# Performance work log

Measured on AMD Instinct MI355X. Metric: run time of the kernel, lower is better.

Reference implementation:

```python
import jax, jax.numpy as jnp
import numpy as np

B, T, U, K, CDIM, S, M = 128, 600, 96, 10, 80, 512, 20
D1 = 3 + CDIM        # rnn1 input: x_t (3) + attention window w (CDIM)
D2 = 3 + S + CDIM    # rnn2 / rnn3 input: x_t + prev rnn out + w
OUT_DIM = 1 + 6 * M


def setup_inputs() -> dict:
    key = jax.random.key(0)
    ks = jax.random.split(key, 16)
    g = lambda k, shape: jax.random.normal(k, shape, jnp.float32) * 0.05
    z = lambda n: jnp.zeros((n,), jnp.float32)
    return {
        "x": jax.random.normal(ks[0], (B, T, 3), jnp.float32),
        "c_vec": jax.random.uniform(ks[1], (B, U, CDIM), jnp.float32),
        # FF cell 1 (input dim D1)
        "W_jx1": g(ks[2], (D1, S)), "b_jx1": z(S),
        "W_jh1": g(ks[3], (S, S)),  "b_jh1": z(S),
        "W_kx1": g(ks[4], (D1, S)), "b_kx1": z(S),
        "W_kh1": g(ks[5], (S, S)),  "b_kh1": z(S),
        # FF cell 2 (input dim D2) -- also used for the 3rd RNN (source reuses self.rnn2)
        "W_jx2": g(ks[6], (D2, S)), "b_jx2": z(S),
        "W_jh2": g(ks[7], (S, S)),  "b_jh2": z(S),
        "W_kx2": g(ks[8], (D2, S)), "b_kx2": z(S),
        "W_kh2": g(ks[9], (S, S)),  "b_kh2": z(S),
        # attention window head: S -> 3K
        "W_win": g(ks[10], (S, 3 * K)), "b_win": z(3 * K),
        # output head: S -> 1 + 6M
        "W_lin": g(ks[11], (S, OUT_DIM)), "b_lin": z(OUT_DIM),
    }


def _ff(inp, h, Wjx, bjx, Wjh, bjh, Wkx, bkx, Wkh, bkh):
    # custom gated cell: out = j*(1-h) + (1-k)*h
    j = jax.nn.sigmoid(inp @ Wjx + bjx + h @ Wjh + bjh)
    k = jax.nn.sigmoid(inp @ Wkx + bkx + h @ Wkh + bkh)
    return j * (1.0 - h) + (1.0 - k) * h


def reference(x, c_vec,
              W_jx1, b_jx1, W_jh1, b_jh1, W_kx1, b_kx1, W_kh1, b_kh1,
              W_jx2, b_jx2, W_jh2, b_jh2, W_kx2, b_kx2, W_kh2, b_kh2,
              W_win, b_win, W_lin, b_lin):
    u = jnp.arange(U, dtype=x.dtype)  # [U]

    def step(carry, xt):
        h1, h2, h3, kappa, w = carry  # h*: [B,S], kappa: [B,K], w: [B,CDIM]
        in1 = jnp.concatenate([xt, w], axis=-1)
        h1 = _ff(in1, h1, W_jx1, b_jx1, W_jh1, b_jh1, W_kx1, b_kx1, W_kh1, b_kh1)
        kg = h1 @ W_win + b_win                       # [B, 3K]
        a_hat, be_hat, k_hat = jnp.split(kg, 3, axis=1)
        alpha = jnp.exp(a_hat)                        # [B,K]
        beta = jnp.exp(be_hat)
        kappa = kappa + jnp.exp(k_hat)
        # phi[b,u] = sum_k alpha * exp(-beta * (kappa - u)^2)
        phi = jnp.sum(alpha[:, :, None] *
                      jnp.exp(-beta[:, :, None] * (kappa[:, :, None] - u) ** 2),
                      axis=1)                          # [B,U]
        w = jnp.einsum('bu,buc->bc', phi, c_vec)      # [B,CDIM]
        in2 = jnp.concatenate([xt, h1, w], axis=-1)
        h2 = _ff(in2, h2, W_jx2, b_jx2, W_jh2, b_jh2, W_kx2, b_kx2, W_kh2, b_kh2)
        in3 = jnp.concatenate([xt, h2, w], axis=-1)
        # source bug kept faithfully: third RNN reuses rnn2's weights
        h3 = _ff(in3, h3, W_jx2, b_jx2, W_jh2, b_jh2, W_kx2, b_kx2, W_kh2, b_kh2)
        return (h1, h2, h3, kappa, w), h3

    zS = jnp.zeros((B, S), x.dtype)
    init = (zS, zS, zS, jnp.zeros((B, K), x.dtype), jnp.zeros((B, CDIM), x.dtype))
    _, ys = jax.lax.scan(step, init, jnp.swapaxes(x, 0, 1))  # ys: [T,B,S]
    out_cat = jnp.swapaxes(ys, 0, 1).reshape(B * T, S)
    return out_cat @ W_lin + b_lin                    # [B*T, 1+6M]
```

## Files before the change

kernel.cpp:

```cpp
#include <hip/hip_runtime.h>
#include <hip/hip_bf16.h>

typedef __bf16 bf16;
typedef __bf16 bf16x8 __attribute__((ext_vector_type(8)));
typedef float  f32x4  __attribute__((ext_vector_type(4)));

#define AS1 __attribute__((address_space(1)))
#define AS3 __attribute__((address_space(3)))

#define NT   600
#define NB   128
#define NS   512
#define NU   96
#define NK   10
#define NC   80
#define NOUT 121

#define W1X_J 0
#define W1W_J 16384
#define W1H_J 65536
#define W1X_K 327680
#define W1W_K 344064
#define W1H_K 393216
#define W2X_J 655360
#define W2W_J 671744
#define W2A_J 720896
#define W2H_J 983040
#define W2X_K 1245184
#define W2W_K 1261568
#define W2A_K 1310720
#define W2H_K 1572864
#define WWIN  1835008
#define WLIN  1851392

#define BIAS_BYTE_OFF 3833856
#define H_BYTE_OFF    3842048
#define HBUF 65536
#define FLAG_BYTE_OFF 4659200
#define BAR_BYTE_OFF  4659264

#define HSTRIDE 520

#define AUX_SC0   1
#define AUX_SC0S1 17

__device__ __forceinline__ float ldIn(const void* q, long i, int isF32) {
  if (isF32) return ((const float*)q)[i];
  return (float)((const bf16*)q)[i];
}

struct KParams {
  const void* x;
  const void* c_vec;
  const void* b_win;
  const void* b_lin;
  const bf16* W;
  const float* bias;
  bf16* h1; bf16* h2; bf16* h3;
  void* out;
  const int* flag;
  int* bar;
};

template <int AUX>
__device__ __forceinline__ void stage_tile_async(const bf16* g, bf16* lds, int tid) {
  const int w = tid >> 6, lane = tid & 63;
#pragma unroll
  for (int r = 0; r < 4; ++r) {
    const int row = (w << 2) + r;
    __builtin_amdgcn_global_load_lds(
        (const AS1 void*)(g + (size_t)row * NS + (size_t)lane * 8),
        (AS3 void*)(lds + (size_t)row * HSTRIDE), 16, 0, AUX);
  }
}

__device__ __forceinline__ void group_arrive(int* gb) {
  __syncthreads();
  if (threadIdx.x == 0) {
    if ((__hip_atomic_fetch_add(gb, 1, __ATOMIC_RELAXED, __HIP_MEMORY_SCOPE_AGENT) & 31) == 31)
      __hip_atomic_fetch_add(gb + 8, 1, __ATOMIC_RELAXED, __HIP_MEMORY_SCOPE_AGENT);
  }
}
__device__ __forceinline__ void group_wait(int* gb, int target) {
  if (threadIdx.x == 0) {
    while (__hip_atomic_load(gb + 8, __ATOMIC_RELAXED, __HIP_MEMORY_SCOPE_AGENT) < target)
      __builtin_amdgcn_s_sleep(1);
  }
  __syncthreads();
  __atomic_signal_fence(__ATOMIC_ACQ_REL);
}

__device__ __forceinline__ void storeH(unsigned* dst, unsigned v, bool fast) {
  if (fast) *dst = v;
  else __hip_atomic_store(dst, v, __ATOMIC_RELAXED, __HIP_MEMORY_SCOPE_AGENT);
}

__global__ void sniff_kernel(const unsigned short* w, int* flag) {
  __shared__ int cnt;
  if (threadIdx.x == 0) cnt = 0;
  __syncthreads();
  int c = 0;
  for (int i = threadIdx.x; i < 8192; i += 256) {
    unsigned e = (w[2 * i] >> 7) & 0xFF;
    if (e == 0xFF || e < 96) c++;
  }
  atomicAdd(&cnt, c);
  __syncthreads();
  if (threadIdx.x == 0) *flag = (cnt > 512) ? 1 : 0;
}

__global__ void prep_kernel(const void* Wjx1, const void* Wjh1, const void* Wkx1, const void* Wkh1,
                            const void* Wjx2, const void* Wjh2, const void* Wkx2, const void* Wkh2,
                            const void* Wwin, const void* Wlin,
                            const void* bjx1, const void* bjh1, const void* bkx1, const void* bkh1,
                            const void* bjx2, const void* bjh2, const void* bkx2, const void* bkh2,
                            bf16* W, float* bias,
                            bf16* h1, bf16* h2, bf16* h3, int* bar,
                            const int* flag) {
  const int isF32 = *flag;
  const int r = blockIdx.y;
  const int e = blockIdx.x * 256 + threadIdx.x;
  if (r == 16) {
    if (e < 512) {
      bias[e]        = ldIn(bjx1, e, isF32) + ldIn(bjh1, e, isF32);
      bias[512 + e]  = ldIn(bkx1, e, isF32) + ldIn(bkh1, e, isF32);
      bias[1024 + e] = ldIn(bjx2, e, isF32) + ldIn(bjh2, e, isF32);
      bias[1536 + e] = ldIn(bkx2, e, isF32) + ldIn(bkh2, e, isF32);
    }
    return;
  }
  if (r == 17) {
    if (e < HBUF) {
      h1[e] = (bf16)0.f; h1[HBUF + e] = (bf16)0.f;
      h2[e] = (bf16)0.f; h2[HBUF + e] = (bf16)0.f;
      h3[e] = (bf16)0.f; h3[HBUF + e] = (bf16)0.f;
    }
    if (e < 1024) bar[e] = 0;
    return;
  }
  const int   row0s[16]  = {0,3,0, 0,3,0, 0,515,3,0, 0,515,3,0, 0,0};
  const int   klens[16]  = {3,80,512, 3,80,512, 3,80,512,512, 3,80,512,512, 512,512};
  const int   kpads[16]  = {32,96,512, 32,96,512, 32,96,512,512, 32,96,512,512, 512,512};
  const int   cpads[16]  = {512,512,512, 512,512,512, 512,512,512,512, 512,512,512,512, 32,128};
  const int   nsrcs[16]  = {512,512,512, 512,512,512, 512,512,512,512, 512,512,512,512, 30,121};
  const long  offs[16]   = {W1X_J,W1W_J,W1H_J, W1X_K,W1W_K,W1H_K,
                            W2X_J,W2W_J,W2A_J,W2H_J, W2X_K,W2W_K,W2A_K,W2H_K, WWIN,WLIN};
  const void* srcs[16]   = {Wjx1,Wjx1,Wjh1, Wkx1,Wkx1,Wkh1,
                            Wjx2,Wjx2,Wjx2,Wjh2, Wkx2,Wkx2,Wkx2,Wkh2, Wwin,Wlin};
  const int Kpad = kpads[r], cp = cpads[r];
  const long tot = (long)Kpad * cp;
  if (e >= tot) return;
  const int j    = e & 7;
  const int lane = (e >> 3) & 63;
  const int rest = e >> 9;
  const int kbs  = Kpad >> 5;
  const int kb   = rest % kbs;
  const int slab = rest / kbs;
  const int col  = slab * 16 + (lane & 15);
  const int k    = kb * 32 + ((lane >> 4) << 3) + j;
  const int Klen = klens[r], row0 = row0s[r], N = nsrcs[r];
  bf16 v = (bf16)0.f;
  if (k < Klen && col < N) v = (bf16)ldIn(srcs[r], (long)(row0 + k) * N + col, isF32);
  W[offs[r] + e] = v;
}

__device__ __forceinline__ void accum_term(f32x4& acc, int& cnt, int kh,
    const bf16* Arow, int astride, const bf16* B, int kbs,
    int lr, int ko, int lane) {
  for (int kb = 0; kb < kbs; ++kb) {
    if (((cnt++) & 1) != kh) continue;
    bf16x8 a = *(const bf16x8*)(Arow + (size_t)lr * astride + kb * 32 + ko);
    bf16x8 b = *(const bf16x8*)(B + ((size_t)kb * 64 + lane) * 8);
    acc = __builtin_amdgcn_mfma_f32_16x16x32_bf16(a, b, acc, 0, 0, 0);
  }
}

__device__ __forceinline__ void accStore(float* d, const f32x4& a) {
  d[0] = a[0]; d[1] = a[1]; d[2] = a[2]; d[3] = a[3];
}

__global__ __launch_bounds__(256) void scan_kernel(KParams p) {
  const int isF32 = *p.flag;
  const int tid  = threadIdx.x;
  const int wid  = tid >> 6;
  const int lane = tid & 63;
  const int wg   = blockIdx.x;
  const int m    = wg & 7;
  const int slab = wg >> 3;
  const int m16  = m << 4;
  const int lr   = lane & 15;
  const int ko   = (lane >> 4) << 3;
  const int g    = wid >> 1;
  const int kh   = wid & 1;

  unsigned* hg1w = (unsigned*)p.h1;
  unsigned* hg2w = (unsigned*)p.h2;
  unsigned* hg3w = (unsigned*)p.h3;

  __shared__ alignas(16) bf16 wLds[32768];
  __shared__ alignas(16) bf16 h1L[16 * HSTRIDE];
  __shared__ alignas(16) bf16 h2L[16 * HSTRIDE];
  __shared__ alignas(16) bf16 h3L[16 * HSTRIDE];
  __shared__ alignas(16) bf16 xtR[4][16][32];
  __shared__ alignas(16) bf16 wR[3][16][96];
  __shared__ float kapL[16][NK];
  __shared__ float alphaL[16][NK];
  __shared__ float betaL[16][NK];
  __shared__ float phiL[16][NU];
  __shared__ float accA[4][64][5];
  __shared__ float accB[4][64][5];
  __shared__ bf16  hOut1[16][16];
  __shared__ bf16  hOut2[16][16];
  __shared__ bf16  hOut3[16][16];

  for (int i = tid; i < 4 * 16 * 32; i += 256) (&xtR[0][0][0])[i] = (bf16)0.f;
  for (int i = tid; i < 3 * 16 * 96; i += 256) (&wR[0][0][0])[i] = (bf16)0.f;
  for (int i = tid; i < 16 * NK; i += 256) (&kapL[0][0])[i] = 0.f;

  const size_t oX2 = g ? W2X_K : W2X_J, oW2 = g ? W2W_K : W2W_J;
  const size_t oX1 = g ? W1X_K : W1X_J, oW1 = g ? W1W_K : W1W_J, oH1 = g ? W1H_K : W1H_J;
  const bf16* wA2 = wLds + (g ? 8192 : 0);
  const bf16* wH2 = wLds + (g ? 24576 : 16384);

  {
    const bf16* wsrc[4] = { p.W + W2A_J + (size_t)slab * (16 * NS),
                            p.W + W2A_K + (size_t)slab * (16 * NS),
                            p.W + W2H_J + (size_t)slab * (16 * NS),
                            p.W + W2H_K + (size_t)slab * (16 * NS) };
#pragma unroll
    for (int mt = 0; mt < 4; ++mt) {
#pragma unroll
      for (int r = 0; r < 4; ++r) {
        const int chunk = (wid << 2) + r;
        __builtin_amdgcn_global_load_lds(
            (const AS1 void*)(wsrc[mt] + chunk * 512 + lane * 8),
            (AS3 void*)(wLds + mt * 8192 + chunk * 512), 16, 0, 0);
      }
    }
  }
  if (tid < 48) {
    int row = tid / 3, d = tid - row * 3;
    xtR[0][row][d] = (bf16)ldIn(p.x, ((long)(m16 + row) * NT + 0) * 3 + d, isF32);
  }
  __syncthreads();

  int* gb = p.bar + m * 64;
  {
    int xcc = __builtin_amdgcn_s_getreg((3 << 11) | (0 << 6) | 20) & 31;
    if (tid == 0) {
      __hip_atomic_fetch_or((unsigned*)(gb + 32), 1u << xcc,
                            __ATOMIC_RELAXED, __HIP_MEMORY_SCOPE_AGENT);
      __threadfence();
      if ((__hip_atomic_fetch_add(gb + 16, 1, __ATOMIC_RELAXED, __HIP_MEMORY_SCOPE_AGENT) & 31) == 31)
        __hip_atomic_fetch_add(gb + 24, 1, __ATOMIC_RELAXED, __HIP_MEMORY_SCOPE_AGENT);
      while (__hip_atomic_load(gb + 24, __ATOMIC_RELAXED, __HIP_MEMORY_SCOPE_AGENT) < 1)
        __builtin_amdgcn_s_sleep(1);
    }
    __syncthreads();
  }
  const unsigned msk = __hip_atomic_load((unsigned*)(gb + 32),
                                         __ATOMIC_RELAXED, __HIP_MEMORY_SCOPE_AGENT);
  const bool fast = (msk & (msk - 1)) == 0;

  f32x4 acc2pre = {0.f, 0.f, 0.f, 0.f};
  int bt = 0;

  {
    f32x4 acc = {0.f, 0.f, 0.f, 0.f};
    int cnt = 0;
    accum_term(acc, cnt, kh, &xtR[0][0][0], 32, p.W + oX1 + (size_t)slab * NS,       1, lr, ko, lane);
    accum_term(acc, cnt, kh, &wR[0][0][0],  96, p.W + oW1 + (size_t)slab * (3 * NS), 3, lr, ko, lane);
    accStore(accB[wid][lane], acc);
    __syncthreads();
    {
      int ls = tid & 63, r = tid >> 6;
      int s = (slab << 4) + (ls & 15);
      int rowIdx = ((ls >> 4) << 2) + r;
      float jp = accB[0][ls][r] + accB[1][ls][r] + p.bias[0 + s];
      float jj = 1.f / (1.f + __expf(-jp));
      hOut1[rowIdx][ls & 15] = (bf16)jj;
    }
    __syncthreads();
    if (tid < 128) {
      int row = tid >> 3, c = tid & 7;
      union { unsigned u; unsigned short s[2]; } v;
      union { bf16 b; unsigned short s; } a0, a1;
      a0.b = hOut1[row][2 * c]; a1.b = hOut1[row][2 * c + 1];
      v.s[0] = a0.s; v.s[1] = a1.s;
      storeH(hg1w + (m16 + row) * 256 + slab * 8 + c, v.u, fast);
    }
    ++bt;
    group_arrive(gb);
    group_wait(gb, bt);
  }

  for (int i = 0; i <= NT + 2; ++i) {
    const bool A1  = (i <= NT - 1);
    const bool AF1 = (i <= NT - 2);
    const bool A2  = (i >= 1 && i <= NT);
    const bool A3  = (i >= 2 && i <= NT + 1);
    const bool AO  = (i >= 3) && (slab < 8);
    const bool APRE = (i <= NT - 1);

    if (i >= 1 && i <= NT + 1) {
      const bf16* g2 = p.h2 + (size_t)(i & 1) * HBUF + (size_t)m16 * NS;
      if (fast) stage_tile_async<AUX_SC0>(g2, h2L, tid);
      else      stage_tile_async<AUX_SC0S1>(g2, h2L, tid);
    }
    if (i >= 2) {
      const bf16* g3 = p.h3 + (size_t)((i + 1) & 1) * HBUF + (size_t)m16 * NS;
      if (fast) stage_tile_async<AUX_SC0>(g3, h3L, tid);
      else      stage_tile_async<AUX_SC0S1>(g3, h3L, tid);
    }
    if (i <= NT - 2 && tid < 48) {
      int row = tid / 3, d = tid - row * 3;
      xtR[(i + 1) & 3][row][d] = (bf16)ldIn(p.x, ((long)(m16 + row) * NT + (i + 1)) * 3 + d, isF32);
    }
    __syncthreads();

    if (A2) {
      f32x4 acc = acc2pre;
      int cnt = 20;
      accum_term(acc, cnt, kh, h2L, HSTRIDE, wH2, 16, lr, ko, lane);
      accStore(accA[wid][lane], acc);
    }
    if (AO) {
      f32x4 acc = {0.f, 0.f, 0.f, 0.f};
      const bf16* B = p.W + WLIN + (size_t)slab * (16 * NS);
      for (int kb = 0; kb < 16; ++kb) {
        if ((kb & 3) != wid) continue;
        bf16x8 a = *(const bf16x8*)(h3L + (size_t)lr * HSTRIDE + kb * 32 + ko);
        bf16x8 b = *(const bf16x8*)(B + ((size_t)kb * 64 + lane) * 8);
        acc = __builtin_amdgcn_mfma_f32_16x16x32_bf16(a, b, acc, 0, 0, 0);
      }
      accStore(accB[wid][lane], acc);
    }
    __syncthreads();

    if (A2) {
      int ls = tid & 63, r = tid >> 6;
      int s = (slab << 4) + (ls & 15);
      int rowIdx = ((ls >> 4) << 2) + r;
      float jp = accA[0][ls][r] + accA[1][ls][r] + p.bias[1024 + s];
      float kp = accA[2][ls][r] + accA[3][ls][r] + p.bias[1536 + s];
      float ho = (float)h2L[rowIdx * HSTRIDE + s];
      float jj = 1.f / (1.f + __expf(-jp));
      float kk = 1.f / (1.f + __expf(-kp));
      hOut2[rowIdx][ls & 15] = (bf16)(jj * (1.f - ho) + (1.f - kk) * ho);
    }
    if (AO && tid < 64) {
      int o = (slab << 4) + (tid & 15);
      if (o < NOUT) {
        float bl = ldIn(p.b_lin, o, isF32);
        int rb = (tid >> 4) << 2;
        for (int r = 0; r < 4; ++r) {
          float v = accB[0][tid][r] + accB[1][tid][r] + accB[2][tid][r] + accB[3][tid][r] + bl;
          long oi = ((long)(m16 + rb + r) * NT + (i - 3)) * NOUT + o;
          if (isF32) ((float*)p.out)[oi] = v; else ((bf16*)p.out)[oi] = (bf16)v;
        }
      }
    }
    __syncthreads();

    if (A3) {
      f32x4 acc = {0.f, 0.f, 0.f, 0.f};
      int cnt = 0;
      accum_term(acc, cnt, kh, &xtR[(i - 2) & 3][0][0], 32, p.W + oX2 + (size_t)slab * NS,      1,  lr, ko, lane);
      accum_term(acc, cnt, kh, h2L, HSTRIDE, wA2, 16, lr, ko, lane);
      accum_term(acc, cnt, kh, &wR[(i - 2) % 3][0][0], 96, p.W + oW2 + (size_t)slab * (3 * NS), 3,  lr, ko, lane);
      accum_term(acc, cnt, kh, h3L, HSTRIDE, wH2, 16, lr, ko, lane);
      accStore(accA[wid][lane], acc);
    }
    if (A2 && tid < 128) {
      int row = tid >> 3, c = tid & 7;
      union { unsigned u; unsigned short s[2]; } v;
      union { bf16 b; unsigned short s; } a0, a1;
      a0.b = hOut2[row][2 * c]; a1.b = hOut2[row][2 * c + 1];
      v.s[0] = a0.s; v.s[1] = a1.s;
      storeH(hg2w + (size_t)((i - 1) & 1) * (HBUF / 2) + (m16 + row) * 256 + slab * 8 + c, v.u, fast);
    }
    __syncthreads();

    if (A3) {
      int ls = tid & 63, r = tid >> 6;
      int s = (slab << 4) + (ls & 15);
      int rowIdx = ((ls >> 4) << 2) + r;
      float jp = accA[0][ls][r] + accA[1][ls][r] + p.bias[1024 + s];
      float kp = accA[2][ls][r] + accA[3][ls][r] + p.bias[1536 + s];
      float ho = (float)h3L[rowIdx * HSTRIDE + s];
      float jj = 1.f / (1.f + __expf(-jp));
      float kk = 1.f / (1.f + __expf(-kp));
      hOut3[rowIdx][ls & 15] = (bf16)(jj * (1.f - ho) + (1.f - kk) * ho);
    }
    __syncthreads();

    if (A1) {
      const bf16* g1 = p.h1 + (size_t)(i & 1) * HBUF + (size_t)m16 * NS;
      if (fast) stage_tile_async<AUX_SC0>(g1, h1L, tid);
      else      stage_tile_async<AUX_SC0S1>(g1, h1L, tid);
    }
    if (A3 && tid < 128) {
      int row = tid >> 3, c = tid & 7;
      union { unsigned u; unsigned short s[2]; } v;
      union { bf16 b; unsigned short s; } a0, a1;
      a0.b = hOut3[row][2 * c]; a1.b = hOut3[row][2 * c + 1];
      v.s[0] = a0.s; v.s[1] = a1.s;
      storeH(hg3w + (size_t)((i - 2) & 1) * (HBUF / 2) + (m16 + row) * 256 + slab * 8 + c, v.u, fast);
    }
    __syncthreads();

    if (A1) {
      int n2 = wid & 1, kh2 = wid >> 1;
      f32x4 acc = {0.f, 0.f, 0.f, 0.f};
      const bf16* B = p.W + WWIN + (size_t)n2 * (16 * NS);
      for (int kb = 0; kb < 16; ++kb) {
        if ((kb & 1) != kh2) continue;
        bf16x8 a = *(const bf16x8*)(h1L + (size_t)lr * HSTRIDE + kb * 32 + ko);
        bf16x8 b = *(const bf16x8*)(B + ((size_t)kb * 64 + lane) * 8);
        acc = __builtin_amdgcn_mfma_f32_16x16x32_bf16(a, b, acc, 0, 0, 0);
      }
      accStore(accA[wid][lane], acc);
    }
    __syncthreads();

    {
      int arow = tid >> 4, aj = tid & 15;
      float lo = 1e30f, hi = -1e30f;
      if (A1 && aj < NK) {
        const int rr = arow & 3;
        const int lbase = (arow >> 2) << 4;
        const int o0 = aj, o1 = NK + aj, o2 = 2 * NK + aj;
        float ah    = accA[o0 >> 4][lbase | (o0 & 15)][rr] + accA[(o0 >> 4) + 2][lbase | (o0 & 15)][rr]
                    + ldIn(p.b_win, o0, isF32);
        float bepre = accA[o1 >> 4][lbase | (o1 & 15)][rr] + accA[(o1 >> 4) + 2][lbase | (o1 & 15)][rr]
                    + ldIn(p.b_win, o1, isF32);
        float dkpre = accA[o2 >> 4][lbase | (o2 & 15)][rr] + accA[(o2 >> 4) + 2][lbase | (o2 & 15)][rr]
                    + ldIn(p.b_win, o2, isF32);
        float be = expf(bepre);
        float dk = expf(dkpre);
        float al = expf(ah);
        float kap = kapL[arow][aj] + dk;
        kapL[arow][aj] = kap;
        alphaL[arow][aj] = al;
        betaL[arow][aj] = be;
        float arg = (ah + 18.42f) / be;
        if (arg > 0.f) { float R = sqrtf(arg); lo = kap - R; hi = kap + R; }
      }
      lo = fminf(lo, __shfl_xor(lo, 1));  hi = fmaxf(hi, __shfl_xor(hi, 1));
      lo = fminf(lo, __shfl_xor(lo, 2));  hi = fmaxf(hi, __shfl_xor(hi, 2));
      lo = fminf(lo, __shfl_xor(lo, 4));  hi = fmaxf(hi, __shfl_xor(hi, 4));
      lo = fminf(lo, __shfl_xor(lo, 8));  hi = fmaxf(hi, __shfl_xor(hi, 8));
      const int ulo = (lo <= 0.f) ? 0 : ((lo > 95.f) ? 96 : (int)floorf(lo));
      const int uhi = (hi >= 95.f) ? 95 : ((hi < 0.f) ? -1 : (int)ceilf(hi));
      __syncthreads();
      if (A1) {
        for (int u = ulo + aj; u <= uhi; u += 16) {
          float s = 0.f, uf = (float)u;
          for (int k2 = 0; k2 < NK; ++k2) {
            float d = kapL[arow][k2] - uf;
            s += alphaL[arow][k2] * __expf(-betaL[arow][k2] * d * d);
          }
          phiL[arow][u] = s;
        }
      }
      __syncthreads();
      if (A1) {
        bf16* wOut = &wR[i % 3][0][0];
        if (isF32) {
          const float* cv = (const float*)p.c_vec + (long)(m16 + arow) * NU * NC;
          for (int ch = aj; ch < 20; ch += 16) {
            float a0 = 0.f, a1 = 0.f, a2 = 0.f, a3 = 0.f;
            for (int u = ulo; u <= uhi; ++u) {
              const float* q = cv + (long)u * NC + (ch << 2);
              float ph = phiL[arow][u];
              a0 += ph * q[0]; a1 += ph * q[1]; a2 += ph * q[2]; a3 += ph * q[3];
            }
            wOut[arow * 96 + (ch << 2) + 0] = (bf16)a0;
            wOut[arow * 96 + (ch << 2) + 1] = (bf16)a1;
            wOut[arow * 96 + (ch << 2) + 2] = (bf16)a2;
            wOut[arow * 96 + (ch << 2) + 3] = (bf16)a3;
          }
        } else {
          const long cv0 = (long)(m16 + arow) * NU * NC;
          for (int c = aj; c < NC; c += 16) {
            float acc = 0.f;
            for (int u = ulo; u <= uhi; ++u)
              acc += phiL[arow][u] * ldIn(p.c_vec, cv0 + (long)u * NC + c, isF32);
            wOut[arow * 96 + c] = (bf16)acc;
          }
        }
      }
    }
    __syncthreads();

    if (AF1) {
      f32x4 acc = {0.f, 0.f, 0.f, 0.f};
      int cnt = 0;
      accum_term(acc, cnt, kh, &xtR[(i + 1) & 3][0][0], 32, p.W + oX1 + (size_t)slab * NS,      1,  lr, ko, lane);
      accum_term(acc, cnt, kh, &wR[i % 3][0][0], 96, p.W + oW1 + (size_t)slab * (3 * NS),       3,  lr, ko, lane);
      accum_term(acc, cnt, kh, h1L, HSTRIDE, p.W + oH1 + (size_t)slab * (16 * NS), 16, lr, ko, lane);
      accStore(accB[wid][lane], acc);
    }
    __syncthreads();

    if (AF1) {
      int ls = tid & 63, r = tid >> 6;
      int s = (slab << 4) + (ls & 15);
      int rowIdx = ((ls >> 4) << 2) + r;
      float jp = accB[0][ls][r] + accB[1][ls][r] + p.bias[0 + s];
      float kp = accB[2][ls][r] + accB[3][ls][r] + p.bias[512 + s];
      float ho = (float)h1L[rowIdx * HSTRIDE + s];
      float jj = 1.f / (1.f + __expf(-jp));
      float kk = 1.f / (1.f + __expf(-kp));
      hOut1[rowIdx][ls & 15] = (bf16)(jj * (1.f - ho) + (1.f - kk) * ho);
    }
    __syncthreads();
    if (AF1 && tid < 128) {
      int row = tid >> 3, c = tid & 7;
      union { unsigned u; unsigned short s[2]; } v;
      union { bf16 b; unsigned short s; } a0, a1;
      a0.b = hOut1[row][2 * c]; a1.b = hOut1[row][2 * c + 1];
      v.s[0] = a0.s; v.s[1] = a1.s;
      storeH(hg1w + (size_t)((i + 1) & 1) * (HBUF / 2) + (m16 + row) * 256 + slab * 8 + c, v.u, fast);
    }

    if (i < NT + 2) {
      ++bt;
      group_arrive(gb);
      if (APRE) {
        f32x4 a = {0.f, 0.f, 0.f, 0.f};
        int cnt = 0;
        accum_term(a, cnt, kh, &xtR[i & 3][0][0], 32, p.W + oX2 + (size_t)slab * NS,      1,  lr, ko, lane);
        accum_term(a, cnt, kh, h1L, HSTRIDE, wA2, 16, lr, ko, lane);
        accum_term(a, cnt, kh, &wR[i % 3][0][0], 96, p.W + oW2 + (size_t)slab * (3 * NS), 3,  lr, ko, lane);
        acc2pre = a;
      }
      group_wait(gb, bt);
    }
  }
}

extern "C" void kernel_launch(void* const* d_in, const int* in_sizes, int n_in,
                              void* d_out, int out_size, void* d_ws, size_t ws_size,
                              hipStream_t stream) {
  (void)in_sizes; (void)n_in; (void)out_size; (void)ws_size;

  bf16*  wsW  = (bf16*)d_ws;
  float* bias = (float*)((char*)d_ws + BIAS_BYTE_OFF);
  bf16*  h1   = (bf16*)((char*)d_ws + H_BYTE_OFF);
  bf16*  h2   = h1 + 2 * HBUF;
  bf16*  h3   = h2 + 2 * HBUF;
  int*   flag = (int*)((char*)d_ws + FLAG_BYTE_OFF);
  int*   bar  = (int*)((char*)d_ws + BAR_BYTE_OFF);

  sniff_kernel<<<1, 256, 0, stream>>>((const unsigned short*)d_in[4], flag);

  prep_kernel<<<dim3(1024, 18), 256, 0, stream>>>(
      d_in[2], d_in[4], d_in[6], d_in[8], d_in[10], d_in[12], d_in[14], d_in[16],
      d_in[18], d_in[20],
      d_in[3], d_in[5], d_in[7], d_in[9], d_in[11], d_in[13], d_in[15], d_in[17],
      wsW, bias, h1, h2, h3, bar, flag);

  KParams kp;
  kp.x = d_in[0]; kp.c_vec = d_in[1]; kp.b_win = d_in[19]; kp.b_lin = d_in[21];
  kp.W = wsW; kp.bias = bias;
  kp.h1 = h1; kp.h2 = h2; kp.h3 = h3;
  kp.out = d_out;
  kp.flag = flag;
  kp.bar = bar;

  scan_kernel<<<256, 256, 0, stream>>>(kp);
}
```

Measured before the change: 10.44 ms.

## Merge per-step phases to cut block barriers and overlap output projection with group wait

```diff
diff --git a/kernel.cpp b/kernel.cpp
--- a/kernel.cpp
+++ b/kernel.cpp
@@ -209,6 +209,7 @@
   __shared__ float phiL[16][NU];
   __shared__ float accA[4][64][5];
   __shared__ float accB[4][64][5];
+  __shared__ float accC[4][64][5];
   __shared__ bf16  hOut1[16][16];
   __shared__ bf16  hOut2[16][16];
   __shared__ bf16  hOut3[16][16];
@@ -312,6 +313,11 @@
       if (fast) stage_tile_async<AUX_SC0>(g3, h3L, tid);
       else      stage_tile_async<AUX_SC0S1>(g3, h3L, tid);
     }
+    if (A1) {
+      const bf16* g1 = p.h1 + (size_t)(i & 1) * HBUF + (size_t)m16 * NS;
+      if (fast) stage_tile_async<AUX_SC0>(g1, h1L, tid);
+      else      stage_tile_async<AUX_SC0S1>(g1, h1L, tid);
+    }
     if (i <= NT - 2 && tid < 48) {
       int row = tid / 3, d = tid - row * 3;
       xtR[(i + 1) & 3][row][d] = (bf16)ldIn(p.x, ((long)(m16 + row) * NT + (i + 1)) * 3 + d, isF32);
@@ -324,44 +330,6 @@
       accum_term(acc, cnt, kh, h2L, HSTRIDE, wH2, 16, lr, ko, lane);
       accStore(accA[wid][lane], acc);
     }
-    if (AO) {
-      f32x4 acc = {0.f, 0.f, 0.f, 0.f};
-      const bf16* B = p.W + WLIN + (size_t)slab * (16 * NS);
-      for (int kb = 0; kb < 16; ++kb) {
-        if ((kb & 3) != wid) continue;
-        bf16x8 a = *(const bf16x8*)(h3L + (size_t)lr * HSTRIDE + kb * 32 + ko);
-        bf16x8 b = *(const bf16x8*)(B + ((size_t)kb * 64 + lane) * 8);
-        acc = __builtin_amdgcn_mfma_f32_16x16x32_bf16(a, b, acc, 0, 0, 0);
-      }
-      accStore(accB[wid][lane], acc);
-    }
-    __syncthreads();
-
-    if (A2) {
-      int ls = tid & 63, r = tid >> 6;
-      int s = (slab << 4) + (ls & 15);
-      int rowIdx = ((ls >> 4) << 2) + r;
-      float jp = accA[0][ls][r] + accA[1][ls][r] + p.bias[1024 + s];
-      float kp = accA[2][ls][r] + accA[3][ls][r] + p.bias[1536 + s];
-      float ho = (float)h2L[rowIdx * HSTRIDE + s];
-      float jj = 1.f / (1.f + __expf(-jp));
-      float kk = 1.f / (1.f + __expf(-kp));
-      hOut2[rowIdx][ls & 15] = (bf16)(jj * (1.f - ho) + (1.f - kk) * ho);
-    }
-    if (AO && tid < 64) {
-      int o = (slab << 4) + (tid & 15);
-      if (o < NOUT) {
-        float bl = ldIn(p.b_lin, o, isF32);
-        int rb = (tid >> 4) << 2;
-        for (int r = 0; r < 4; ++r) {
-          float v = accB[0][tid][r] + accB[1][tid][r] + accB[2][tid][r] + accB[3][tid][r] + bl;
-          long oi = ((long)(m16 + rb + r) * NT + (i - 3)) * NOUT + o;
-          if (isF32) ((float*)p.out)[oi] = v; else ((bf16*)p.out)[oi] = (bf16)v;
-        }
-      }
-    }
-    __syncthreads();
-
     if (A3) {
       f32x4 acc = {0.f, 0.f, 0.f, 0.f};
       int cnt = 0;
@@ -369,46 +337,8 @@
       accum_term(acc, cnt, kh, h2L, HSTRIDE, wA2, 16, lr, ko, lane);
       accum_term(acc, cnt, kh, &wR[(i - 2) % 3][0][0], 96, p.W + oW2 + (size_t)slab * (3 * NS), 3,  lr, ko, lane);
       accum_term(acc, cnt, kh, h3L, HSTRIDE, wH2, 16, lr, ko, lane);
-      accStore(accA[wid][lane], acc);
-    }
-    if (A2 && tid < 128) {
-      int row = tid >> 3, c = tid & 7;
-      union { unsigned u; unsigned short s[2]; } v;
-      union { bf16 b; unsigned short s; } a0, a1;
-      a0.b = hOut2[row][2 * c]; a1.b = hOut2[row][2 * c + 1];
-      v.s[0] = a0.s; v.s[1] = a1.s;
-      storeH(hg2w + (size_t)((i - 1) & 1) * (HBUF / 2) + (m16 + row) * 256 + slab * 8 + c, v.u, fast);
-    }
-    __syncthreads();
-
-    if (A3) {
-      int ls = tid & 63, r = tid >> 6;
-      int s = (slab << 4) + (ls & 15);
-      int rowIdx = ((ls >> 4) << 2) + r;
-      float jp = accA[0][ls][r] + accA[1][ls][r] + p.bias[1024 + s];
-      float kp = accA[2][ls][r] + accA[3][ls][r] + p.bias[1536 + s];
-      float ho = (float)h3L[rowIdx * HSTRIDE + s];
-      float jj = 1.f / (1.f + __expf(-jp));
-      float kk = 1.f / (1.f + __expf(-kp));
-      hOut3[rowIdx][ls & 15] = (bf16)(jj * (1.f - ho) + (1.f - kk) * ho);
-    }
-    __syncthreads();
-
-    if (A1) {
-      const bf16* g1 = p.h1 + (size_t)(i & 1) * HBUF + (size_t)m16 * NS;
-      if (fast) stage_tile_async<AUX_SC0>(g1, h1L, tid);
-      else      stage_tile_async<AUX_SC0S1>(g1, h1L, tid);
-    }
-    if (A3 && tid < 128) {
-      int row = tid >> 3, c = tid & 7;
-      union { unsigned u; unsigned short s[2]; } v;
-      union { bf16 b; unsigned short s; } a0, a1;
-      a0.b = hOut3[row][2 * c]; a1.b = hOut3[row][2 * c + 1];
-      v.s[0] = a0.s; v.s[1] = a1.s;
-      storeH(hg3w + (size_t)((i - 2) & 1) * (HBUF / 2) + (m16 + row) * 256 + slab * 8 + c, v.u, fast);
-    }
-    __syncthreads();
-
+      accStore(accC[wid][lane], acc);
+    }
     if (A1) {
       int n2 = wid & 1, kh2 = wid >> 1;
       f32x4 acc = {0.f, 0.f, 0.f, 0.f};
@@ -419,22 +349,45 @@
         bf16x8 b = *(const bf16x8*)(B + ((size_t)kb * 64 + lane) * 8);
         acc = __builtin_amdgcn_mfma_f32_16x16x32_bf16(a, b, acc, 0, 0, 0);
       }
-      accStore(accA[wid][lane], acc);
-    }
-    __syncthreads();
-
+      accStore(accB[wid][lane], acc);
+    }
+    __syncthreads();
+
+    const int arow = tid >> 4, aj = tid & 15;
+    int ulo, uhi;
     {
-      int arow = tid >> 4, aj = tid & 15;
+      if (A2) {
+        int ls = tid & 63, r = tid >> 6;
+        int s = (slab << 4) + (ls & 15);
+        int rowIdx = ((ls >> 4) << 2) + r;
+        float jp = accA[0][ls][r] + accA[1][ls][r] + p.bias[1024 + s];
+        float kp = accA[2][ls][r] + accA[3][ls][r] + p.bias[1536 + s];
+        float ho = (float)h2L[rowIdx * HSTRIDE + s];
+        float jj = 1.f / (1.f + __expf(-jp));
+        float kk = 1.f / (1.f + __expf(-kp));
+        hOut2[rowIdx][ls & 15] = (bf16)(jj * (1.f - ho) + (1.f - kk) * ho);
+      }
+      if (A3) {
+        int ls = tid & 63, r = tid >> 6;
+        int s = (slab << 4) + (ls & 15);
+        int rowIdx = ((ls >> 4) << 2) + r;
+        float jp = accC[0][ls][r] + accC[1][ls][r] + p.bias[1024 + s];
+        float kp = accC[2][ls][r] + accC[3][ls][r] + p.bias[1536 + s];
+        float ho = (float)h3L[rowIdx * HSTRIDE + s];
+        float jj = 1.f / (1.f + __expf(-jp));
+        float kk = 1.f / (1.f + __expf(-kp));
+        hOut3[rowIdx][ls & 15] = (bf16)(jj * (1.f - ho) + (1.f - kk) * ho);
+      }
       float lo = 1e30f, hi = -1e30f;
       if (A1 && aj < NK) {
         const int rr = arow & 3;
         const int lbase = (arow >> 2) << 4;
         const int o0 = aj, o1 = NK + aj, o2 = 2 * NK + aj;
-        float ah    = accA[o0 >> 4][lbase | (o0 & 15)][rr] + accA[(o0 >> 4) + 2][lbase | (o0 & 15)][rr]
+        float ah    = accB[o0 >> 4][lbase | (o0 & 15)][rr] + accB[(o0 >> 4) + 2][lbase | (o0 & 15)][rr]
                     + ldIn(p.b_win, o0, isF32);
-        float bepre = accA[o1 >> 4][lbase | (o1 & 15)][rr] + accA[(o1 >> 4) + 2][lbase | (o1 & 15)][rr]
+        float bepre = accB[o1 >> 4][lbase | (o1 & 15)][rr] + accB[(o1 >> 4) + 2][lbase | (o1 & 15)][rr]
                     + ldIn(p.b_win, o1, isF32);
-        float dkpre = accA[o2 >> 4][lbase | (o2 & 15)][rr] + accA[(o2 >> 4) + 2][lbase | (o2 & 15)][rr]
+        float dkpre = accB[o2 >> 4][lbase | (o2 & 15)][rr] + accB[(o2 >> 4) + 2][lbase | (o2 & 15)][rr]
                     + ldIn(p.b_win, o2, isF32);
         float be = expf(bepre);
         float dk = expf(dkpre);
@@ -450,44 +403,63 @@
       lo = fminf(lo, __shfl_xor(lo, 2));  hi = fmaxf(hi, __shfl_xor(hi, 2));
       lo = fminf(lo, __shfl_xor(lo, 4));  hi = fmaxf(hi, __shfl_xor(hi, 4));
       lo = fminf(lo, __shfl_xor(lo, 8));  hi = fmaxf(hi, __shfl_xor(hi, 8));
-      const int ulo = (lo <= 0.f) ? 0 : ((lo > 95.f) ? 96 : (int)floorf(lo));
-      const int uhi = (hi >= 95.f) ? 95 : ((hi < 0.f) ? -1 : (int)ceilf(hi));
-      __syncthreads();
-      if (A1) {
-        for (int u = ulo + aj; u <= uhi; u += 16) {
-          float s = 0.f, uf = (float)u;
-          for (int k2 = 0; k2 < NK; ++k2) {
-            float d = kapL[arow][k2] - uf;
-            s += alphaL[arow][k2] * __expf(-betaL[arow][k2] * d * d);
+      ulo = (lo <= 0.f) ? 0 : ((lo > 95.f) ? 96 : (int)floorf(lo));
+      uhi = (hi >= 95.f) ? 95 : ((hi < 0.f) ? -1 : (int)ceilf(hi));
+    }
+    __syncthreads();
+
+    if (A1) {
+      for (int u = ulo + aj; u <= uhi; u += 16) {
+        float s = 0.f, uf = (float)u;
+        for (int k2 = 0; k2 < NK; ++k2) {
+          float d = kapL[arow][k2] - uf;
+          s += alphaL[arow][k2] * __expf(-betaL[arow][k2] * d * d);
+        }
+        phiL[arow][u] = s;
+      }
+    }
+    if (A2 && tid < 128) {
+      int row = tid >> 3, c = tid & 7;
+      union { unsigned u; unsigned short s[2]; } v;
+      union { bf16 b; unsigned short s; } a0, a1;
+      a0.b = hOut2[row][2 * c]; a1.b = hOut2[row][2 * c + 1];
+      v.s[0] = a0.s; v.s[1] = a1.s;
+      storeH(hg2w + (size_t)((i - 1) & 1) * (HBUF / 2) + (m16 + row) * 256 + slab * 8 + c, v.u, fast);
+    }
+    if (A3 && tid >= 128) {
+      int t2 = tid - 128;
+      int row = t2 >> 3, c = t2 & 7;
+      union { unsigned u; unsigned short s[2]; } v;
+      union { bf16 b; unsigned short s; } a0, a1;
+      a0.b = hOut3[row][2 * c]; a1.b = hOut3[row][2 * c + 1];
+      v.s[0] = a0.s; v.s[1] = a1.s;
+      storeH(hg3w + (size_t)((i - 2) & 1) * (HBUF / 2) + (m16 + row) * 256 + slab * 8 + c, v.u, fast);
+    }
+    __syncthreads();
+
+    if (A1) {
+      bf16* wOut = &wR[i % 3][0][0];
+      if (isF32) {
+        const float* cv = (const float*)p.c_vec + (long)(m16 + arow) * NU * NC;
+        for (int ch = aj; ch < 20; ch += 16) {
+          float a0 = 0.f, a1 = 0.f, a2 = 0.f, a3 = 0.f;
+          for (int u = ulo; u <= uhi; ++u) {
+            const float* q = cv + (long)u * NC + (ch << 2);
+            float ph = phiL[arow][u];
+            a0 += ph * q[0]; a1 += ph * q[1]; a2 += ph * q[2]; a3 += ph * q[3];
           }
-          phiL[arow][u] = s;
+          wOut[arow * 96 + (ch << 2) + 0] = (bf16)a0;
+          wOut[arow * 96 + (ch << 2) + 1] = (bf16)a1;
+          wOut[arow * 96 + (ch << 2) + 2] = (bf16)a2;
+          wOut[arow * 96 + (ch << 2) + 3] = (bf16)a3;
         }
-      }
-      __syncthreads();
-      if (A1) {
-        bf16* wOut = &wR[i % 3][0][0];
-        if (isF32) {
-          const float* cv = (const float*)p.c_vec + (long)(m16 + arow) * NU * NC;
-          for (int ch = aj; ch < 20; ch += 16) {
-            float a0 = 0.f, a1 = 0.f, a2 = 0.f, a3 = 0.f;
-            for (int u = ulo; u <= uhi; ++u) {
-              const float* q = cv + (long)u * NC + (ch << 2);
-              float ph = phiL[arow][u];
-              a0 += ph * q[0]; a1 += ph * q[1]; a2 += ph * q[2]; a3 += ph * q[3];
-            }
-            wOut[arow * 96 + (ch << 2) + 0] = (bf16)a0;
-            wOut[arow * 96 + (ch << 2) + 1] = (bf16)a1;
-            wOut[arow * 96 + (ch << 2) + 2] = (bf16)a2;
-            wOut[arow * 96 + (ch << 2) + 3] = (bf16)a3;
-          }
-        } else {
-          const long cv0 = (long)(m16 + arow) * NU * NC;
-          for (int c = aj; c < NC; c += 16) {
-            float acc = 0.f;
-            for (int u = ulo; u <= uhi; ++u)
-              acc += phiL[arow][u] * ldIn(p.c_vec, cv0 + (long)u * NC + c, isF32);
-            wOut[arow * 96 + c] = (bf16)acc;
-          }
+      } else {
+        const long cv0 = (long)(m16 + arow) * NU * NC;
+        for (int c = aj; c < NC; c += 16) {
+          float acc = 0.f;
+          for (int u = ulo; u <= uhi; ++u)
+            acc += phiL[arow][u] * ldIn(p.c_vec, cv0 + (long)u * NC + c, isF32);
+          wOut[arow * 96 + c] = (bf16)acc;
         }
       }
     }
@@ -515,6 +487,7 @@
       hOut1[rowIdx][ls & 15] = (bf16)(jj * (1.f - ho) + (1.f - kk) * ho);
     }
     __syncthreads();
+
     if (AF1 && tid < 128) {
       int row = tid >> 3, c = tid & 7;
       union { unsigned u; unsigned short s[2]; } v;
@@ -523,20 +496,43 @@
       v.s[0] = a0.s; v.s[1] = a1.s;
       storeH(hg1w + (size_t)((i + 1) & 1) * (HBUF / 2) + (m16 + row) * 256 + slab * 8 + c, v.u, fast);
     }
-
-    if (i < NT + 2) {
-      ++bt;
-      group_arrive(gb);
-      if (APRE) {
-        f32x4 a = {0.f, 0.f, 0.f, 0.f};
-        int cnt = 0;
-        accum_term(a, cnt, kh, &xtR[i & 3][0][0], 32, p.W + oX2 + (size_t)slab * NS,      1,  lr, ko, lane);
-        accum_term(a, cnt, kh, h1L, HSTRIDE, wA2, 16, lr, ko, lane);
-        accum_term(a, cnt, kh, &wR[i % 3][0][0], 96, p.W + oW2 + (size_t)slab * (3 * NS), 3,  lr, ko, lane);
-        acc2pre = a;
-      }
-      group_wait(gb, bt);
-    }
+    if (i < NT + 2) { ++bt; group_arrive(gb); }
+    else            __syncthreads();
+    if (APRE) {
+      f32x4 a = {0.f, 0.f, 0.f, 0.f};
+      int cnt = 0;
+      accum_term(a, cnt, kh, &xtR[i & 3][0][0], 32, p.W + oX2 + (size_t)slab * NS,      1,  lr, ko, lane);
+      accum_term(a, cnt, kh, h1L, HSTRIDE, wA2, 16, lr, ko, lane);
+      accum_term(a, cnt, kh, &wR[i % 3][0][0], 96, p.W + oW2 + (size_t)slab * (3 * NS), 3,  lr, ko, lane);
+      acc2pre = a;
+    }
+    if (AO) {
+      f32x4 acc = {0.f, 0.f, 0.f, 0.f};
+      const bf16* B = p.W + WLIN + (size_t)slab * (16 * NS);
+      for (int kb = 0; kb < 16; ++kb) {
+        if ((kb & 3) != wid) continue;
+        bf16x8 a = *(const bf16x8*)(h3L + (size_t)lr * HSTRIDE + kb * 32 + ko);
+        bf16x8 b = *(const bf16x8*)(B + ((size_t)kb * 64 + lane) * 8);
+        acc = __builtin_amdgcn_mfma_f32_16x16x32_bf16(a, b, acc, 0, 0, 0);
+      }
+      accStore(accA[wid][lane], acc);
+    }
+    if (i >= 3 && slab < 8) {
+      __syncthreads();
+      if (tid < 64) {
+        int o = (slab << 4) + (tid & 15);
+        if (o < NOUT) {
+          float bl = ldIn(p.b_lin, o, isF32);
+          int rb = (tid >> 4) << 2;
+          for (int r = 0; r < 4; ++r) {
+            float v = accA[0][tid][r] + accA[1][tid][r] + accA[2][tid][r] + accA[3][tid][r] + bl;
+            long oi = ((long)(m16 + rb + r) * NT + (i - 3)) * NOUT + o;
+            if (isF32) ((float*)p.out)[oi] = v; else ((bf16*)p.out)[oi] = (bf16)v;
+          }
+        }
+      }
+    }
+    if (i < NT + 2) group_wait(gb, bt);
   }
 }
 
```

Result: faster. 9.675 ms (-7.3%).
